# Performance work log

Hardware: AMD Instinct MI355X
Metric: run time of the kernel (lower is better)

Reference implementation:

```python
import jax, jax.numpy as jnp
import numpy as np

N = 100000      # nodes
E = 1600000     # edges
G = 256         # graphs in batch
F_IN = 100      # node_features
H = 64          # hidden_channels
L = 3           # num_conv_layers


def setup_inputs() -> dict:
    key = jax.random.key(0)
    ks = jax.random.split(key, 16)
    def w(k, shape, fan_in):
        return (jax.random.normal(k, shape, jnp.float32) / np.sqrt(fan_in)).astype(jnp.float32)
    return {
        "x": jax.random.normal(ks[0], (N, F_IN), jnp.float32),
        "edge_index": jax.random.randint(ks[1], (2, E), 0, N, dtype=jnp.int32),
        "batch": jnp.sort(jax.random.randint(ks[2], (N,), 0, G, dtype=jnp.int32)),
        "W_emb": w(ks[3], (F_IN, H), F_IN),
        "b_emb": jnp.zeros((H,), jnp.float32),
        "conv_W": w(ks[4], (L, H, H), H),
        "conv_b": jnp.zeros((L, H), jnp.float32),
        "W1": w(ks[5], (H, H), H),
        "b1": jnp.zeros((H,), jnp.float32),
        "W2": w(ks[6], (H, H // 2), H),
        "b2": jnp.zeros((H // 2,), jnp.float32),
        "W3": w(ks[7], (H // 2, 1), H // 2),
        "b3": jnp.zeros((1,), jnp.float32),
    }


def reference(x, edge_index, batch, W_emb, b_emb, conv_W, conv_b, W1, b1, W2, b2, W3, b3):
    # --- GCN normalization with self-loops (PyG GCNConv defaults) ---
    loop = jnp.arange(N, dtype=edge_index.dtype)
    src = jnp.concatenate([edge_index[0], loop])  # [E+N]
    dst = jnp.concatenate([edge_index[1], loop])  # [E+N]
    deg = jax.ops.segment_sum(jnp.ones_like(dst, jnp.float32), dst, num_segments=N)
    dinv = jax.lax.rsqrt(jnp.maximum(deg, 1.0))   # deg >= 1 because of self-loops
    norm = dinv[src] * dinv[dst]                   # [E+N]

    # --- embed ---
    h = jax.nn.relu(x @ W_emb + b_emb)             # [N, H]

    # --- stacked GCNConv: h' = scatter_add(norm * (hW)[src] -> dst) + b ---
    for i in range(conv_W.shape[0]):
        hw = h @ conv_W[i]                          # [N, H]
        msg = hw[src] * norm[:, None]               # [E+N, H] gather + scale
        agg = jax.ops.segment_sum(msg, dst, num_segments=N)
        h = jax.nn.relu(agg + conv_b[i])

    # --- global mean pool over batch ids ---
    cnt = jax.ops.segment_sum(jnp.ones((N,), jnp.float32), batch, num_segments=G)
    pooled = jax.ops.segment_sum(h, batch, num_segments=G) / jnp.maximum(cnt, 1.0)[:, None]

    # --- MLP readout 64 -> 64 -> 32 -> 1 ---
    r = jax.nn.relu(pooled @ W1 + b1)
    r = jax.nn.relu(r @ W2 + b2)
    return r @ W3 + b3                              # [G, 1]
```

## Files before the change

kernel.cpp:

```cpp
#include <hip/hip_runtime.h>
#include <hip/hip_bf16.h>

#define NN 100000
#define NE 1600000
#define NG 256
#define FIN 100
#define HH 64

#define BSHIFT 8
#define BSIZE 256
#define NBUCK ((NN + BSIZE - 1) / BSIZE)
#define BCAP 4608
#define CHUNK 4096
#define NPLACE ((NE + CHUNK - 1) / CHUNK)

#define NBLK64 ((NN + 63) / 64)
#define AGGB (NN / 32)

#define SXE 136
#define SH 72

typedef __attribute__((ext_vector_type(8))) short short8;
typedef __attribute__((ext_vector_type(4))) float f32x4;

__device__ __forceinline__ float relu_f(float x){ return x > 0.f ? x : 0.f; }
__device__ __forceinline__ unsigned short f2b(float f) {
    unsigned int u = __float_as_uint(f);
    u += 0x7fffu + ((u >> 16) & 1u);
    return (unsigned short)(u >> 16);
}
__device__ __forceinline__ unsigned pk2(float a, float b) {
    return (unsigned)f2b(a) | ((unsigned)f2b(b) << 16);
}
__device__ __forceinline__ float b2f(unsigned short h) {
    return __uint_as_float(((unsigned int)h) << 16);
}
__device__ __forceinline__ float lo32(unsigned u){ return __uint_as_float(u << 16); }
__device__ __forceinline__ float hi32(unsigned u){ return __uint_as_float(u & 0xffff0000u); }

__global__ __launch_bounds__(256) void k_prep(const float* __restrict__ Wemb,
                                              const float* __restrict__ convW,
                                              unsigned short* __restrict__ WeT,
                                              unsigned short* __restrict__ WcT,
                                              int* __restrict__ bucket_cnt) {
    int t = threadIdx.x;
    for (int i = t; i < NBUCK; i += 256) bucket_cnt[i] = 0;
    for (int i = t; i < 64 * 128; i += 256) WeT[i] = 0;
    __syncthreads();
    for (int i = t; i < FIN * HH; i += 256) {
        int k = i >> 6, n = i & 63;
        WeT[n * 128 + k] = f2b(Wemb[i]);
    }
    for (int l = 0; l < 3; ++l)
        for (int i = t; i < HH * HH; i += 256) {
            int k = i >> 6, n = i & 63;
            WcT[l * 4096 + n * 64 + k] = f2b(convW[l * 4096 + i]);
        }
}

__global__ __launch_bounds__(256) void k_bplace(const int* __restrict__ src,
                                                const int* __restrict__ dst,
                                                int* __restrict__ bucket_cnt,
                                                unsigned int* __restrict__ upairs) {
    __shared__ int h[NBUCK];
    __shared__ int base[NBUCK];
    int t = threadIdx.x;
    for (int i = t; i < NBUCK; i += 256) h[i] = 0;
    __syncthreads();
    int e0 = blockIdx.x * CHUNK;
    int e1 = e0 + CHUNK; if (e1 > NE) e1 = NE;
    for (int i = e0 + t; i < e1; i += 256) atomicAdd(&h[dst[i] >> BSHIFT], 1);
    __syncthreads();
    for (int i = t; i < NBUCK; i += 256) {
        int c = h[i];
        base[i] = c ? atomicAdd(&bucket_cnt[i], c) : 0;
    }
    __syncthreads();
    for (int i = t; i < NBUCK; i += 256) h[i] = 0;
    __syncthreads();
    for (int i = e0 + t; i < e1; i += 256) {
        int d = dst[i];
        int b = d >> BSHIFT;
        int pos = b * BCAP + base[b] + atomicAdd(&h[b], 1);
        upairs[pos] = ((unsigned)(d & (BSIZE - 1)) << 17) | (unsigned)src[i];
    }
}

__global__ __launch_bounds__(256) void k_csr_embed(const int* __restrict__ bucket_cnt,
                                                   const unsigned int* __restrict__ upairs,
                                                   int* __restrict__ row_start,
                                                   unsigned short* __restrict__ deg16,
                                                   float* __restrict__ dinv,
                                                   int* __restrict__ csr_src,
                                                   const float* __restrict__ x,
                                                   const unsigned short* __restrict__ WeT,
                                                   const float* __restrict__ bemb,
                                                   const unsigned short* __restrict__ W0T,
                                                   unsigned short* __restrict__ g0) {
    __shared__ int degl[BSIZE];
    __shared__ int curl[BSIZE];
    __shared__ int wsum4[4];
    __shared__ __align__(16) unsigned short Xl[64 * SXE];
    int t = threadIdx.x;
    int lane = t & 63, w = t >> 6;

    if (blockIdx.x < NBUCK) {
        int b = blockIdx.x;
        int nbase = b << BSHIFT;
        int ncnt = NN - nbase; if (ncnt > BSIZE) ncnt = BSIZE;
        for (int i = t; i < BSIZE; i += 256) degl[i] = 0;
        __syncthreads();
        int p0 = b * BCAP;
        int p1 = p0 + bucket_cnt[b];
        for (int i = p0 + t; i < p1; i += 256) atomicAdd(&degl[upairs[i] >> 17], 1);
        __syncthreads();
        int vseg = degl[w * 64 + lane];
        int inc = vseg;
        for (int off = 1; off < 64; off <<= 1) {
            int n = __shfl_up(inc, off, 64);
            if (lane >= off) inc += n;
        }
        if (lane == 63) wsum4[w] = inc;
        __syncthreads();
        int soff = 0;
        for (int s = 0; s < w; ++s) soff += wsum4[s];
        int idx = w * 64 + lane;
        int rs = p0 + soff + inc - vseg;
        curl[idx] = rs;
        if (idx < ncnt) {
            row_start[nbase + idx] = rs;
            deg16[nbase + idx] = (unsigned short)vseg;
            dinv[nbase + idx] = rsqrtf((float)(vseg + 1));
        }
        __syncthreads();
        for (int i = p0 + t; i < p1; i += 256) {
            unsigned pk = upairs[i];
            int pos = atomicAdd(&curl[pk >> 17], 1);
            csr_src[pos] = (int)(pk & 0x1FFFFu);
        }
        return;
    }

    int row0 = (blockIdx.x - NBUCK) * 64;
    unsigned* Xl32 = (unsigned*)Xl;
    for (int i = t; i < 64 * 25; i += 256) {
        int r = i / 25, q = i - r * 25;
        int row = row0 + r;
        uint2 pkd = {0u, 0u};
        if (row < NN) {
            float4 xv = *reinterpret_cast<const float4*>(&x[(size_t)row * FIN + q * 4]);
            pkd.x = pk2(xv.x, xv.y);
            pkd.y = pk2(xv.z, xv.w);
        }
        *reinterpret_cast<uint2*>(&Xl[r * SXE + q * 4]) = pkd;
    }
    for (int i = t; i < 64 * 18; i += 256) {
        int r = i / 18, q = i - r * 18;
        Xl32[r * 68 + 50 + q] = 0u;
    }
    __syncthreads();
    int m16 = lane & 15, g4 = lane >> 4;
    f32x4 acc[4] = {{0,0,0,0},{0,0,0,0},{0,0,0,0},{0,0,0,0}};
    const unsigned short* Arow = &Xl[(w * 16 + m16) * SXE + g4 * 8];
    #pragma unroll
    for (int kk = 0; kk < 4; ++kk) {
        short8 a = *reinterpret_cast<const short8*>(Arow + kk * 32);
        #pragma unroll
        for (int c = 0; c < 4; ++c) {
            short8 bf = *reinterpret_cast<const short8*>(&WeT[(size_t)(c * 16 + m16) * 128 + g4 * 8 + kk * 32]);
            acc[c] = __builtin_amdgcn_mfma_f32_16x16x32_bf16(a, bf, acc[c], 0, 0, 0);
        }
    }
    __syncthreads();
    unsigned short* hl = Xl;
    #pragma unroll
    for (int c = 0; c < 4; ++c) {
        int col = c * 16 + m16;
        float bb = bemb[col];
        #pragma unroll
        for (int r = 0; r < 4; ++r) {
            int rr = w * 16 + g4 * 4 + r;
            hl[rr * SH + col] = f2b(relu_f(acc[c][r] + bb));
        }
    }
    __syncthreads();
    f32x4 acc2[4] = {{0,0,0,0},{0,0,0,0},{0,0,0,0},{0,0,0,0}};
    const unsigned short* Hrow = &hl[(w * 16 + m16) * SH + g4 * 8];
    #pragma unroll
    for (int kk = 0; kk < 2; ++kk) {
        short8 a = *reinterpret_cast<const short8*>(Hrow + kk * 32);
        #pragma unroll
        for (int c = 0; c < 4; ++c) {
            short8 bf = *reinterpret_cast<const short8*>(&W0T[(size_t)(c * 16 + m16) * 64 + g4 * 8 + kk * 32]);
            acc2[c] = __builtin_amdgcn_mfma_f32_16x16x32_bf16(a, bf, acc2[c], 0, 0, 0);
        }
    }
    __syncthreads();
    #pragma unroll
    for (int c = 0; c < 4; ++c) {
        int col = c * 16 + m16;
        #pragma unroll
        for (int r = 0; r < 4; ++r) {
            int rr = w * 16 + g4 * 4 + r;
            hl[rr * SH + col] = f2b(acc2[c][r]);
        }
    }
    __syncthreads();
    for (int i = t; i < 64 * 8; i += 256) {
        int r = i >> 3, c8 = i & 7;
        int row = row0 + r;
        if (row < NN)
            *reinterpret_cast<uint4*>(&g0[(size_t)row * HH + c8 * 8]) =
                *reinterpret_cast<const uint4*>(&Xl[r * SH + c8 * 8]);
    }
}

template <int ES, int GEMM>
__global__ __launch_bounds__(256) void k_agg(const int* __restrict__ row_start,
                                             const unsigned short* __restrict__ deg16,
                                             const int* __restrict__ csr_src,
                                             const unsigned short* __restrict__ g,
                                             const float* __restrict__ dinv,
                                             const float* __restrict__ bL,
                                             const unsigned short* __restrict__ WT,
                                             unsigned short* __restrict__ outbuf) {
    __shared__ __align__(16) unsigned short hl[32 * SH];
    int t = threadIdx.x;
    int lane = t & 63, w = t >> 6;
    int oct = lane >> 3;
    int sub = lane & 7;
    int v0 = blockIdx.x * 32;
    int v = v0 + w * 8 + oct;
    int st = row_start[v];
    int n = deg16[v];
    float dvv = dinv[v];
    float a0,a1,a2,a3,a4,a5,a6,a7;
    {
        uint4 u = *reinterpret_cast<const uint4*>(&g[(size_t)v * HH + sub * 8]);
        float sc = ES ? dvv : 1.f;
        a0 = sc*lo32(u.x); a1 = sc*hi32(u.x); a2 = sc*lo32(u.y); a3 = sc*hi32(u.y);
        a4 = sc*lo32(u.z); a5 = sc*hi32(u.z); a6 = sc*lo32(u.w); a7 = sc*hi32(u.w);
    }
    int sb = oct << 3;
    for (int base = 0; base < n; base += 8) {
        int m = n - base; if (m > 8) m = 8;
        int sv = (sub < m) ? csr_src[st + base + sub] : 0;
        float dl = 0.f;
        if (ES) dl = (sub < m) ? dinv[sv] : 0.f;
        int j = 0;
        for (; j + 4 <= m; j += 4) {
            int s0 = __shfl(sv, sb + j),     s1 = __shfl(sv, sb + j + 1);
            int s2 = __shfl(sv, sb + j + 2), s3 = __shfl(sv, sb + j + 3);
            uint4 u0 = *reinterpret_cast<const uint4*>(&g[(size_t)s0 * HH + sub * 8]);
            uint4 u1 = *reinterpret_cast<const uint4*>(&g[(size_t)s1 * HH + sub * 8]);
            uint4 u2 = *reinterpret_cast<const uint4*>(&g[(size_t)s2 * HH + sub * 8]);
            uint4 u3 = *reinterpret_cast<const uint4*>(&g[(size_t)s3 * HH + sub * 8]);
            if (ES) {
                float d0 = __shfl(dl, sb + j),     d1 = __shfl(dl, sb + j + 1);
                float d2 = __shfl(dl, sb + j + 2), d3 = __shfl(dl, sb + j + 3);
                a0 = fmaf(d0, lo32(u0.x), a0); a1 = fmaf(d0, hi32(u0.x), a1);
                a2 = fmaf(d0, lo32(u0.y), a2); a3 = fmaf(d0, hi32(u0.y), a3);
                a4 = fmaf(d0, lo32(u0.z), a4); a5 = fmaf(d0, hi32(u0.z), a5);
                a6 = fmaf(d0, lo32(u0.w), a6); a7 = fmaf(d0, hi32(u0.w), a7);
                a0 = fmaf(d1, lo32(u1.x), a0); a1 = fmaf(d1, hi32(u1.x), a1);
                a2 = fmaf(d1, lo32(u1.y), a2); a3 = fmaf(d1, hi32(u1.y), a3);
                a4 = fmaf(d1, lo32(u1.z), a4); a5 = fmaf(d1, hi32(u1.z), a5);
                a6 = fmaf(d1, lo32(u1.w), a6); a7 = fmaf(d1, hi32(u1.w), a7);
                a0 = fmaf(d2, lo32(u2.x), a0); a1 = fmaf(d2, hi32(u2.x), a1);
                a2 = fmaf(d2, lo32(u2.y), a2); a3 = fmaf(d2, hi32(u2.y), a3);
                a4 = fmaf(d2, lo32(u2.z), a4); a5 = fmaf(d2, hi32(u2.z), a5);
                a6 = fmaf(d2, lo32(u2.w), a6); a7 = fmaf(d2, hi32(u2.w), a7);
                a0 = fmaf(d3, lo32(u3.x), a0); a1 = fmaf(d3, hi32(u3.x), a1);
                a2 = fmaf(d3, lo32(u3.y), a2); a3 = fmaf(d3, hi32(u3.y), a3);
                a4 = fmaf(d3, lo32(u3.z), a4); a5 = fmaf(d3, hi32(u3.z), a5);
                a6 = fmaf(d3, lo32(u3.w), a6); a7 = fmaf(d3, hi32(u3.w), a7);
            } else {
                a0 += lo32(u0.x); a1 += hi32(u0.x); a2 += lo32(u0.y); a3 += hi32(u0.y);
                a4 += lo32(u0.z); a5 += hi32(u0.z); a6 += lo32(u0.w); a7 += hi32(u0.w);
                a0 += lo32(u1.x); a1 += hi32(u1.x); a2 += lo32(u1.y); a3 += hi32(u1.y);
                a4 += lo32(u1.z); a5 += hi32(u1.z); a6 += lo32(u1.w); a7 += hi32(u1.w);
                a0 += lo32(u2.x); a1 += hi32(u2.x); a2 += lo32(u2.y); a3 += hi32(u2.y);
                a4 += lo32(u2.z); a5 += hi32(u2.z); a6 += lo32(u2.w); a7 += hi32(u2.w);
                a0 += lo32(u3.x); a1 += hi32(u3.x); a2 += lo32(u3.y); a3 += hi32(u3.y);
                a4 += lo32(u3.z); a5 += hi32(u3.z); a6 += lo32(u3.w); a7 += hi32(u3.w);
            }
        }
        for (; j < m; ++j) {
            int s = __shfl(sv, sb + j);
            uint4 u = *reinterpret_cast<const uint4*>(&g[(size_t)s * HH + sub * 8]);
            if (ES) {
                float d = __shfl(dl, sb + j);
                a0 = fmaf(d, lo32(u.x), a0); a1 = fmaf(d, hi32(u.x), a1);
                a2 = fmaf(d, lo32(u.y), a2); a3 = fmaf(d, hi32(u.y), a3);
                a4 = fmaf(d, lo32(u.z), a4); a5 = fmaf(d, hi32(u.z), a5);
                a6 = fmaf(d, lo32(u.w), a6); a7 = fmaf(d, hi32(u.w), a7);
            } else {
                a0 += lo32(u.x); a1 += hi32(u.x); a2 += lo32(u.y); a3 += hi32(u.y);
                a4 += lo32(u.z); a5 += hi32(u.z); a6 += lo32(u.w); a7 += hi32(u.w);
            }
        }
    }
    float4 bb0 = *reinterpret_cast<const float4*>(&bL[sub * 8]);
    float4 bb1 = *reinterpret_cast<const float4*>(&bL[sub * 8 + 4]);
    uint4 hv;
    hv.x = pk2(relu_f(dvv * a0 + bb0.x), relu_f(dvv * a1 + bb0.y));
    hv.y = pk2(relu_f(dvv * a2 + bb0.z), relu_f(dvv * a3 + bb0.w));
    hv.z = pk2(relu_f(dvv * a4 + bb1.x), relu_f(dvv * a5 + bb1.y));
    hv.w = pk2(relu_f(dvv * a6 + bb1.z), relu_f(dvv * a7 + bb1.w));
    if (!GEMM) {
        *reinterpret_cast<uint4*>(&outbuf[(size_t)v * HH + sub * 8]) = hv;
        return;
    }
    int lrow = w * 8 + oct;
    *reinterpret_cast<uint4*>(&hl[lrow * SH + sub * 8]) = hv;
    __syncthreads();
    int m16 = lane & 15, g4 = lane >> 4;
    int rb = w & 1, cbase = (w >> 1) * 2;
    f32x4 acc2[2] = {{0,0,0,0},{0,0,0,0}};
    #pragma unroll
    for (int kk = 0; kk < 2; ++kk) {
        short8 a = *reinterpret_cast<const short8*>(&hl[(rb * 16 + m16) * SH + g4 * 8 + kk * 32]);
        #pragma unroll
        for (int c = 0; c < 2; ++c) {
            short8 bf = *reinterpret_cast<const short8*>(&WT[(size_t)((cbase + c) * 16 + m16) * 64 + g4 * 8 + kk * 32]);
            acc2[c] = __builtin_amdgcn_mfma_f32_16x16x32_bf16(a, bf, acc2[c], 0, 0, 0);
        }
    }
    __syncthreads();
    #pragma unroll
    for (int r = 0; r < 4; ++r) {
        int lr = rb * 16 + g4 * 4 + r;
        float dv2 = dinv[v0 + lr];
        #pragma unroll
        for (int c = 0; c < 2; ++c) {
            int col = (cbase + c) * 16 + m16;
            hl[lr * SH + col] = f2b(dv2 * acc2[c][r]);
        }
    }
    __syncthreads();
    {
        int r = t >> 3, c8 = t & 7;
        *reinterpret_cast<uint4*>(&outbuf[(size_t)(v0 + r) * HH + c8 * 8]) =
            *reinterpret_cast<const uint4*>(&hl[r * SH + c8 * 8]);
    }
}

__global__ __launch_bounds__(512) void k_pool_mlp(const unsigned short* __restrict__ h,
                                                  const int* __restrict__ batch,
                                                  const float* __restrict__ W1, const float* __restrict__ b1,
                                                  const float* __restrict__ W2, const float* __restrict__ b2,
                                                  const float* __restrict__ W3, const float* __restrict__ b3,
                                                  float* __restrict__ out) {
    int g = blockIdx.x;
    int lo = 0, hi_s = NN;
    while (lo < hi_s) { int mid = (lo + hi_s) >> 1; if (batch[mid] < g) lo = mid + 1; else hi_s = mid; }
    int lo2 = lo, hi = NN;
    while (lo2 < hi) { int mid = (lo2 + hi) >> 1; if (batch[mid] < g + 1) lo2 = mid + 1; else hi = mid; }
    int lane = threadIdx.x & 63;
    int wave = threadIdx.x >> 6;
    float s = 0.f;
    for (int n = lo + wave; n < hi; n += 8) {
        s += b2f(h[(size_t)n * HH + lane]);
    }
    __shared__ float red[8][64];
    __shared__ float pv[64];
    __shared__ float tv[64];
    __shared__ float qv[32];
    red[wave][lane] = s;
    __syncthreads();
    int cnt = hi - lo;
    float invc = 1.f / (float)(cnt > 0 ? cnt : 1);
    if (threadIdx.x < 64) {
        float acc = 0.f;
        #pragma unroll
        for (int r = 0; r < 8; ++r) acc += red[r][lane];
        pv[lane] = acc * invc;
    }
    __syncthreads();
    if (threadIdx.x < 64) {
        int j = threadIdx.x;
        float s1 = b1[j];
        #pragma unroll
        for (int k = 0; k < 64; ++k) s1 = fmaf(pv[k], W1[k * 64 + j], s1);
        tv[j] = relu_f(s1);
    }
    __syncthreads();
    if (threadIdx.x < 32) {
        int j = threadIdx.x;
        float s2 = b2[j];
        #pragma unroll
        for (int k = 0; k < 64; ++k) s2 = fmaf(tv[k], W2[k * 32 + j], s2);
        qv[j] = relu_f(s2);
    }
    __syncthreads();
    if (threadIdx.x == 0) {
        float s3 = b3[0];
        #pragma unroll
        for (int k = 0; k < 32; ++k) s3 = fmaf(qv[k], W3[k], s3);
        out[g] = s3;
    }
}

extern "C" void kernel_launch(void* const* d_in, const int* in_sizes, int n_in,
                              void* d_out, int out_size, void* d_ws, size_t ws_size,
                              hipStream_t stream) {
    const float* x    = (const float*)d_in[0];
    const int*   ei   = (const int*)d_in[1];
    const int*   batch= (const int*)d_in[2];
    const float* Wemb = (const float*)d_in[3];
    const float* bemb = (const float*)d_in[4];
    const float* convW= (const float*)d_in[5];
    const float* convb= (const float*)d_in[6];
    const float* W1   = (const float*)d_in[7];
    const float* b1   = (const float*)d_in[8];
    const float* W2   = (const float*)d_in[9];
    const float* b2   = (const float*)d_in[10];
    const float* W3   = (const float*)d_in[11];
    const float* b3   = (const float*)d_in[12];
    float* out = (float*)d_out;

    auto alignup = [](size_t v) { return (v + 255) & ~(size_t)255; };
    char* p = (char*)d_ws;
    int*   row_start    = (int*)p;            p += alignup((size_t)NN * 4);
    unsigned short* deg16 = (unsigned short*)p; p += alignup((size_t)NN * 2);
    float* dinv         = (float*)p;          p += alignup((size_t)NN * 4);
    int*   bucket_cnt   = (int*)p;            p += alignup((size_t)NBUCK * 4);
    int*   csr_src      = (int*)p;            p += alignup((size_t)NBUCK * BCAP * 4);
    unsigned short* WeT = (unsigned short*)p; p += alignup((size_t)64 * 128 * 2);
    unsigned short* WcT = (unsigned short*)p; p += alignup((size_t)3 * 4096 * 2);
    unsigned short* bufA = (unsigned short*)p; p += alignup((size_t)NN * HH * 2);
    unsigned short* bufB = (unsigned short*)p; p += alignup((size_t)NN * HH * 2);
    unsigned int* upairs = (unsigned int*)bufB;

    const int* srcA = ei;
    const int* dstA = ei + NE;

    k_prep<<<1, 256, 0, stream>>>(Wemb, convW, WeT, WcT, bucket_cnt);
    k_bplace<<<NPLACE, 256, 0, stream>>>(srcA, dstA, bucket_cnt, upairs);

    k_csr_embed<<<NBUCK + NBLK64, 256, 0, stream>>>(bucket_cnt, upairs, row_start, deg16, dinv,
                                                    csr_src, x, WeT, bemb, WcT + 0 * 4096, bufA);

    k_agg<1,1><<<AGGB, 256, 0, stream>>>(row_start, deg16, csr_src, bufA, dinv,
                                         convb + 0 * HH, WcT + 1 * 4096, bufB);
    k_agg<0,1><<<AGGB, 256, 0, stream>>>(row_start, deg16, csr_src, bufB, dinv,
                                         convb + 1 * HH, WcT + 2 * 4096, bufA);
    k_agg<0,0><<<AGGB, 256, 0, stream>>>(row_start, deg16, csr_src, bufA, dinv,
                                         convb + 2 * HH, nullptr, bufB);

    k_pool_mlp<<<NG, 512, 0, stream>>>(bufB, batch, W1, b1, W2, b2, W3, b3, out);
}
```

Before: 217.7 us.

## Gather eight neighbours per pass with zero-row padding and prefetch next indices

The aggregation loop now always issues eight row gathers per pass, replacing the old 4-wide loop plus scalar tail. Missing neighbours are redirected to an extra all-zero sentinel row appended to each feature buffer and cleared in the prep kernel. The next batch of CSR source indices and their dinv values is loaded while the current batch is processed. The GEMM epilogue writes to a second LDS buffer, which removes one block-wide barrier. The aim is more loads in flight and less index-load latency, at the cost of extra sentinel gathers on partial batches and more registers.

After: 202.2 us. 7.1% less time.

```diff
diff --git a/kernel.cpp b/kernel.cpp
--- a/kernel.cpp
+++ b/kernel.cpp
@@ -38,13 +38,23 @@
 __device__ __forceinline__ float lo32(unsigned u){ return __uint_as_float(u << 16); }
 __device__ __forceinline__ float hi32(unsigned u){ return __uint_as_float(u & 0xffff0000u); }
 
+#define ACC8(U) { a0 += lo32(U.x); a1 += hi32(U.x); a2 += lo32(U.y); a3 += hi32(U.y); \
+                  a4 += lo32(U.z); a5 += hi32(U.z); a6 += lo32(U.w); a7 += hi32(U.w); }
+#define FMA8(D,U) { a0 = fmaf(D, lo32(U.x), a0); a1 = fmaf(D, hi32(U.x), a1); \
+                    a2 = fmaf(D, lo32(U.y), a2); a3 = fmaf(D, hi32(U.y), a3); \
+                    a4 = fmaf(D, lo32(U.z), a4); a5 = fmaf(D, hi32(U.z), a5); \
+                    a6 = fmaf(D, lo32(U.w), a6); a7 = fmaf(D, hi32(U.w), a7); }
+
 __global__ __launch_bounds__(256) void k_prep(const float* __restrict__ Wemb,
                                               const float* __restrict__ convW,
                                               unsigned short* __restrict__ WeT,
                                               unsigned short* __restrict__ WcT,
-                                              int* __restrict__ bucket_cnt) {
+                                              int* __restrict__ bucket_cnt,
+                                              unsigned short* __restrict__ zrowA,
+                                              unsigned short* __restrict__ zrowB) {
     int t = threadIdx.x;
     for (int i = t; i < NBUCK; i += 256) bucket_cnt[i] = 0;
+    if (t < 64) { zrowA[t] = 0; zrowB[t] = 0; }
     for (int i = t; i < 64 * 128; i += 256) WeT[i] = 0;
     __syncthreads();
     for (int i = t; i < FIN * HH; i += 256) {
@@ -224,7 +234,7 @@
                                              const float* __restrict__ bL,
                                              const unsigned short* __restrict__ WT,
                                              unsigned short* __restrict__ outbuf) {
-    __shared__ __align__(16) unsigned short hl[32 * SH];
+    __shared__ __align__(16) unsigned short hls[GEMM ? 2 * 32 * SH : 1];
     int t = threadIdx.x;
     int lane = t & 63, w = t >> 6;
     int oct = lane >> 3;
@@ -242,63 +252,46 @@
         a4 = sc*lo32(u.z); a5 = sc*hi32(u.z); a6 = sc*lo32(u.w); a7 = sc*hi32(u.w);
     }
     int sb = oct << 3;
+    int m0 = n < 8 ? n : 8;
+    int sv = (sub < m0) ? csr_src[st + sub] : 0;
+    float dl = 0.f;
+    if (ES) dl = (sub < m0) ? dinv[sv] : 0.f;
     for (int base = 0; base < n; base += 8) {
-        int m = n - base; if (m > 8) m = 8;
-        int sv = (sub < m) ? csr_src[st + base + sub] : 0;
-        float dl = 0.f;
-        if (ES) dl = (sub < m) ? dinv[sv] : 0.f;
-        int j = 0;
-        for (; j + 4 <= m; j += 4) {
-            int s0 = __shfl(sv, sb + j),     s1 = __shfl(sv, sb + j + 1);
-            int s2 = __shfl(sv, sb + j + 2), s3 = __shfl(sv, sb + j + 3);
-            uint4 u0 = *reinterpret_cast<const uint4*>(&g[(size_t)s0 * HH + sub * 8]);
-            uint4 u1 = *reinterpret_cast<const uint4*>(&g[(size_t)s1 * HH + sub * 8]);
-            uint4 u2 = *reinterpret_cast<const uint4*>(&g[(size_t)s2 * HH + sub * 8]);
-            uint4 u3 = *reinterpret_cast<const uint4*>(&g[(size_t)s3 * HH + sub * 8]);
-            if (ES) {
-                float d0 = __shfl(dl, sb + j),     d1 = __shfl(dl, sb + j + 1);
-                float d2 = __shfl(dl, sb + j + 2), d3 = __shfl(dl, sb + j + 3);
-                a0 = fmaf(d0, lo32(u0.x), a0); a1 = fmaf(d0, hi32(u0.x), a1);
-                a2 = fmaf(d0, lo32(u0.y), a2); a3 = fmaf(d0, hi32(u0.y), a3);
-                a4 = fmaf(d0, lo32(u0.z), a4); a5 = fmaf(d0, hi32(u0.z), a5);
-                a6 = fmaf(d0, lo32(u0.w), a6); a7 = fmaf(d0, hi32(u0.w), a7);
-                a0 = fmaf(d1, lo32(u1.x), a0); a1 = fmaf(d1, hi32(u1.x), a1);
-                a2 = fmaf(d1, lo32(u1.y), a2); a3 = fmaf(d1, hi32(u1.y), a3);
-                a4 = fmaf(d1, lo32(u1.z), a4); a5 = fmaf(d1, hi32(u1.z), a5);
-                a6 = fmaf(d1, lo32(u1.w), a6); a7 = fmaf(d1, hi32(u1.w), a7);
-                a0 = fmaf(d2, lo32(u2.x), a0); a1 = fmaf(d2, hi32(u2.x), a1);
-                a2 = fmaf(d2, lo32(u2.y), a2); a3 = fmaf(d2, hi32(u2.y), a3);
-                a4 = fmaf(d2, lo32(u2.z), a4); a5 = fmaf(d2, hi32(u2.z), a5);
-                a6 = fmaf(d2, lo32(u2.w), a6); a7 = fmaf(d2, hi32(u2.w), a7);
-                a0 = fmaf(d3, lo32(u3.x), a0); a1 = fmaf(d3, hi32(u3.x), a1);
-                a2 = fmaf(d3, lo32(u3.y), a2); a3 = fmaf(d3, hi32(u3.y), a3);
-                a4 = fmaf(d3, lo32(u3.z), a4); a5 = fmaf(d3, hi32(u3.z), a5);
-                a6 = fmaf(d3, lo32(u3.w), a6); a7 = fmaf(d3, hi32(u3.w), a7);
-            } else {
-                a0 += lo32(u0.x); a1 += hi32(u0.x); a2 += lo32(u0.y); a3 += hi32(u0.y);
-                a4 += lo32(u0.z); a5 += hi32(u0.z); a6 += lo32(u0.w); a7 += hi32(u0.w);
-                a0 += lo32(u1.x); a1 += hi32(u1.x); a2 += lo32(u1.y); a3 += hi32(u1.y);
-                a4 += lo32(u1.z); a5 += hi32(u1.z); a6 += lo32(u1.w); a7 += hi32(u1.w);
-                a0 += lo32(u2.x); a1 += hi32(u2.x); a2 += lo32(u2.y); a3 += hi32(u2.y);
-                a4 += lo32(u2.z); a5 += hi32(u2.z); a6 += lo32(u2.w); a7 += hi32(u2.w);
-                a0 += lo32(u3.x); a1 += hi32(u3.x); a2 += lo32(u3.y); a3 += hi32(u3.y);
-                a4 += lo32(u3.z); a5 += hi32(u3.z); a6 += lo32(u3.w); a7 += hi32(u3.w);
-            }
-        }
-        for (; j < m; ++j) {
-            int s = __shfl(sv, sb + j);
-            uint4 u = *reinterpret_cast<const uint4*>(&g[(size_t)s * HH + sub * 8]);
-            if (ES) {
-                float d = __shfl(dl, sb + j);
-                a0 = fmaf(d, lo32(u.x), a0); a1 = fmaf(d, hi32(u.x), a1);
-                a2 = fmaf(d, lo32(u.y), a2); a3 = fmaf(d, hi32(u.y), a3);
-                a4 = fmaf(d, lo32(u.z), a4); a5 = fmaf(d, hi32(u.z), a5);
-                a6 = fmaf(d, lo32(u.w), a6); a7 = fmaf(d, hi32(u.w), a7);
-            } else {
-                a0 += lo32(u.x); a1 += hi32(u.x); a2 += lo32(u.y); a3 += hi32(u.y);
-                a4 += lo32(u.z); a5 += hi32(u.z); a6 += lo32(u.w); a7 += hi32(u.w);
-            }
-        }
+        int mw = n - base; if (mw > 8) mw = 8;
+        int mn = n - base - 8; if (mn > 8) mn = 8;
+        int svn = 0; float dln = 0.f;
+        if (mn > 0) {
+            svn = (sub < mn) ? csr_src[st + base + 8 + sub] : 0;
+            if (ES) dln = (sub < mn) ? dinv[svn] : 0.f;
+        }
+        int s0 = (0 < mw) ? __shfl(sv, sb + 0) : NN;
+        int s1 = (1 < mw) ? __shfl(sv, sb + 1) : NN;
+        int s2 = (2 < mw) ? __shfl(sv, sb + 2) : NN;
+        int s3 = (3 < mw) ? __shfl(sv, sb + 3) : NN;
+        int s4 = (4 < mw) ? __shfl(sv, sb + 4) : NN;
+        int s5 = (5 < mw) ? __shfl(sv, sb + 5) : NN;
+        int s6 = (6 < mw) ? __shfl(sv, sb + 6) : NN;
+        int s7 = (7 < mw) ? __shfl(sv, sb + 7) : NN;
+        uint4 u0 = *reinterpret_cast<const uint4*>(&g[(size_t)s0 * HH + sub * 8]);
+        uint4 u1 = *reinterpret_cast<const uint4*>(&g[(size_t)s1 * HH + sub * 8]);
+        uint4 u2 = *reinterpret_cast<const uint4*>(&g[(size_t)s2 * HH + sub * 8]);
+        uint4 u3 = *reinterpret_cast<const uint4*>(&g[(size_t)s3 * HH + sub * 8]);
+        uint4 u4 = *reinterpret_cast<const uint4*>(&g[(size_t)s4 * HH + sub * 8]);
+        uint4 u5 = *reinterpret_cast<const uint4*>(&g[(size_t)s5 * HH + sub * 8]);
+        uint4 u6 = *reinterpret_cast<const uint4*>(&g[(size_t)s6 * HH + sub * 8]);
+        uint4 u7 = *reinterpret_cast<const uint4*>(&g[(size_t)s7 * HH + sub * 8]);
+        if (ES) {
+            float d0 = __shfl(dl, sb + 0), d1 = __shfl(dl, sb + 1);
+            float d2 = __shfl(dl, sb + 2), d3 = __shfl(dl, sb + 3);
+            float d4 = __shfl(dl, sb + 4), d5 = __shfl(dl, sb + 5);
+            float d6 = __shfl(dl, sb + 6), d7 = __shfl(dl, sb + 7);
+            FMA8(d0, u0); FMA8(d1, u1); FMA8(d2, u2); FMA8(d3, u3);
+            FMA8(d4, u4); FMA8(d5, u5); FMA8(d6, u6); FMA8(d7, u7);
+        } else {
+            ACC8(u0); ACC8(u1); ACC8(u2); ACC8(u3);
+            ACC8(u4); ACC8(u5); ACC8(u6); ACC8(u7);
+        }
+        sv = svn; dl = dln;
     }
     float4 bb0 = *reinterpret_cast<const float4*>(&bL[sub * 8]);
     float4 bb1 = *reinterpret_cast<const float4*>(&bL[sub * 8 + 4]);
@@ -311,6 +304,8 @@
         *reinterpret_cast<uint4*>(&outbuf[(size_t)v * HH + sub * 8]) = hv;
         return;
     }
+    unsigned short* hl = hls;
+    unsigned short* gl = hls + 32 * SH;
     int lrow = w * 8 + oct;
     *reinterpret_cast<uint4*>(&hl[lrow * SH + sub * 8]) = hv;
     __syncthreads();
@@ -326,7 +321,6 @@
             acc2[c] = __builtin_amdgcn_mfma_f32_16x16x32_bf16(a, bf, acc2[c], 0, 0, 0);
         }
     }
-    __syncthreads();
     #pragma unroll
     for (int r = 0; r < 4; ++r) {
         int lr = rb * 16 + g4 * 4 + r;
@@ -334,14 +328,14 @@
         #pragma unroll
         for (int c = 0; c < 2; ++c) {
             int col = (cbase + c) * 16 + m16;
-            hl[lr * SH + col] = f2b(dv2 * acc2[c][r]);
+            gl[lr * SH + col] = f2b(dv2 * acc2[c][r]);
         }
     }
     __syncthreads();
     {
         int r = t >> 3, c8 = t & 7;
         *reinterpret_cast<uint4*>(&outbuf[(size_t)(v0 + r) * HH + c8 * 8]) =
-            *reinterpret_cast<const uint4*>(&hl[r * SH + c8 * 8]);
+            *reinterpret_cast<const uint4*>(&gl[r * SH + c8 * 8]);
     }
 }
 
@@ -428,14 +422,15 @@
     int*   csr_src      = (int*)p;            p += alignup((size_t)NBUCK * BCAP * 4);
     unsigned short* WeT = (unsigned short*)p; p += alignup((size_t)64 * 128 * 2);
     unsigned short* WcT = (unsigned short*)p; p += alignup((size_t)3 * 4096 * 2);
-    unsigned short* bufA = (unsigned short*)p; p += alignup((size_t)NN * HH * 2);
-    unsigned short* bufB = (unsigned short*)p; p += alignup((size_t)NN * HH * 2);
+    unsigned short* bufA = (unsigned short*)p; p += alignup(((size_t)NN * HH + 64) * 2);
+    unsigned short* bufB = (unsigned short*)p; p += alignup(((size_t)NN * HH + 64) * 2);
     unsigned int* upairs = (unsigned int*)bufB;
 
     const int* srcA = ei;
     const int* dstA = ei + NE;
 
-    k_prep<<<1, 256, 0, stream>>>(Wemb, convW, WeT, WcT, bucket_cnt);
+    k_prep<<<1, 256, 0, stream>>>(Wemb, convW, WeT, WcT, bucket_cnt,
+                                  bufA + (size_t)NN * HH, bufB + (size_t)NN * HH);
     k_bplace<<<NPLACE, 256, 0, stream>>>(srcA, dstA, bucket_cnt, upairs);
 
     k_csr_embed<<<NBUCK + NBLK64, 256, 0, stream>>>(bucket_cnt, upairs, row_start, deg16, dinv,
```
